# Optimization experiments

Hardware: AMD Instinct MI355X
Metric: run time of the kernel (lower is better)

Reference implementation:

```python
import jax, jax.numpy as jnp
import numpy as np

USER_NUM = 100000
ITEM_NUM = 50000
N_NODES = USER_NUM + ITEM_NUM
HIDE_DIM = 64
N_EDGES = 4000000
LAYER_NUM = 3


def setup_inputs() -> dict:
    key = jax.random.key(0)
    k1, k2, k3, k4 = jax.random.split(key, 4)
    # Xavier uniform for embeddings: bound = sqrt(6/(fan_in+fan_out))
    bound_u = float(np.sqrt(6.0 / (USER_NUM + HIDE_DIM)))
    bound_i = float(np.sqrt(6.0 / (ITEM_NUM + HIDE_DIM)))
    user_emb = jax.random.uniform(k1, (USER_NUM, HIDE_DIM), jnp.float32, -bound_u, bound_u)
    item_emb = jax.random.uniform(k2, (ITEM_NUM, HIDE_DIM), jnp.float32, -bound_i, bound_i)
    src = jax.random.randint(k3, (N_EDGES,), 0, N_NODES, dtype=jnp.int32)
    dst = jax.random.randint(k4, (N_EDGES,), 0, N_NODES, dtype=jnp.int32)
    return {"user_emb": user_emb, "item_emb": item_emb, "src": src, "dst": dst}


def _gcn_layer(node_f, src, dst, out_norm, in_norm):
    # node_f: [N, D]; symmetric degree-normalized SpMM (copy_u + sum)
    h = node_f * out_norm  # pre-scale by out_degree^-0.5
    agg = jax.ops.segment_sum(h[src], dst, num_segments=N_NODES)
    return agg * in_norm  # post-scale by in_degree^-0.5


def reference(user_emb, item_emb, src, dst):
    ones = jnp.ones((N_EDGES,), jnp.float32)
    out_deg = jnp.clip(jax.ops.segment_sum(ones, src, num_segments=N_NODES), 1.0)
    in_deg = jnp.clip(jax.ops.segment_sum(ones, dst, num_segments=N_NODES), 1.0)
    out_norm = (out_deg ** -0.5)[:, None]
    in_norm = (in_deg ** -0.5)[:, None]

    res_user = user_emb
    res_item = item_emb
    for i in range(LAYER_NUM):
        if i == 0:
            node_f = jnp.concatenate([res_user, res_item], axis=0)
        else:
            node_f = embeddings
        embeddings = _gcn_layer(node_f, src, dst, out_norm, in_norm)
        scale = 1.0 / (i + 2)
        res_user = res_user + embeddings[:USER_NUM] * scale
        res_item = res_item + embeddings[USER_NUM:] * scale
    return (res_user, res_item)
```

## Files before the change

kernel.cpp:

```cpp
#include <hip/hip_runtime.h>
#include <stdint.h>

#define USER_NUM 100000
#define ITEM_NUM 50000
#define N_NODES  150000
#define HIDE_DIM 64
#define N_EDGES  4000000

#define HRANGES 3
#define RNODES  50000
#define RWORDS  (RNODES / 4)
#define SLICES  128
#define EPS     (N_EDGES / SLICES)
#define NRB     ((HRANGES * RWORDS + 511) / 512)

#define BSH     9
#define BNODES  512
#define NBUCK   293
#define SSLICES 640
#define EPSB    (N_EDGES / SSLICES)

#define STAGE_CAP 15000
#define INIT_BLOCKS ((N_NODES * 32) / 512)

__device__ __forceinline__ unsigned short f2bf(float f) {
    union { float f; unsigned int i; } c; c.f = f;
    unsigned int b = c.i;
    return (unsigned short)((b + 0x7FFFu + ((b >> 16) & 1u)) >> 16);
}
__device__ __forceinline__ float lo_bf(uint32_t u) {
    union { uint32_t u; float f; } c; c.u = u << 16; return c.f;
}
__device__ __forceinline__ float hi_bf(uint32_t u) {
    union { uint32_t u; float f; } c; c.u = u & 0xffff0000u; return c.f;
}

__global__ void histfused_kernel(const int* __restrict__ src, const int* __restrict__ dst,
                                 uint32_t* __restrict__ partial, uint32_t* __restrict__ btot) {
    __shared__ uint32_t bins[RWORDS];
    int r  = blockIdx.x / SLICES;
    int sl = blockIdx.x - r * SLICES;
    int e0 = sl * EPS, e1 = e0 + EPS;
    if (r < HRANGES) {
        for (int i = threadIdx.x; i < RWORDS; i += 512) bins[i] = 0;
        __syncthreads();
        int lo = r * RNODES, hi = lo + RNODES;
        for (int e = e0 + threadIdx.x; e < e1; e += 512) {
            int s = src[e];
            if (s >= lo && s < hi) {
                int x = s - lo;
                atomicAdd(&bins[x >> 2], 1u << (8 * (x & 3)));
            }
        }
        __syncthreads();
        uint32_t* out = partial + (size_t)(r * SLICES + sl) * RWORDS;
        for (int i = threadIdx.x; i < RWORDS; i += 512) out[i] = bins[i];
    } else {
        for (int i = threadIdx.x; i < NBUCK; i += 512) bins[i] = 0;
        __syncthreads();
        for (int e = e0 + threadIdx.x; e < e1; e += 512)
            atomicAdd(&bins[((unsigned)dst[e]) >> BSH], 1u);
        __syncthreads();
        for (int i = threadIdx.x; i < NBUCK; i += 512)
            if (bins[i]) atomicAdd(&btot[i], bins[i]);
    }
}

__global__ void rednorm_kernel(const uint32_t* __restrict__ partial, float* __restrict__ out_norm,
                               const uint32_t* __restrict__ btot, uint32_t* __restrict__ bbase) {
    if (blockIdx.x == NRB) {
        __shared__ uint32_t tot[512];
        int t = threadIdx.x;
        uint32_t v = (t < NBUCK) ? btot[t] : 0;
        tot[t] = v;
        __syncthreads();
        for (int off = 1; off < 512; off <<= 1) {
            uint32_t x = (t >= off) ? tot[t - off] : 0;
            __syncthreads();
            tot[t] += x;
            __syncthreads();
        }
        if (t < NBUCK) bbase[t] = tot[t] - v;
        if (t == NBUCK - 1) bbase[NBUCK] = tot[t];
        return;
    }
    int g = blockIdx.x * 512 + threadIdx.x;
    if (g >= HRANGES * RWORDS) return;
    int r = g / RWORDS, w = g - r * RWORDS;
    const uint32_t* p = partial + (size_t)r * SLICES * RWORDS + w;
    uint32_t acc = 0;
#pragma unroll 16
    for (int sl = 0; sl < SLICES; ++sl) acc += p[(size_t)sl * RWORDS];
    int oc0 = acc & 255, oc1 = (acc >> 8) & 255, oc2 = (acc >> 16) & 255, oc3 = (acc >> 24);
    float4 o;
    o.x = 1.0f / sqrtf((float)(oc0 < 1 ? 1 : oc0));
    o.y = 1.0f / sqrtf((float)(oc1 < 1 ? 1 : oc1));
    o.z = 1.0f / sqrtf((float)(oc2 < 1 ? 1 : oc2));
    o.w = 1.0f / sqrtf((float)(oc3 < 1 ? 1 : oc3));
    ((float4*)out_norm)[(size_t)r * (RNODES / 4) + w] = o;
}

__global__ void scatter_kernel(const int* __restrict__ src, const int* __restrict__ dst,
                               const uint32_t* __restrict__ bbase, uint32_t* __restrict__ gcur,
                               uint32_t* __restrict__ sorted) {
    __shared__ uint32_t cnt[NBUCK];
    __shared__ uint32_t excl[NBUCK];
    __shared__ uint32_t gpos0[NBUCK];
    __shared__ uint32_t sarr[512];
    __shared__ uint32_t sval[EPSB];
    __shared__ uint16_t sbkt[EPSB];

    int s = blockIdx.x;
    int t = threadIdx.x;
    for (int i = t; i < NBUCK; i += 512) cnt[i] = 0;
    __syncthreads();

    int e0 = s * EPSB;
    for (int e = e0 + t; e < e0 + EPSB; e += 512)
        atomicAdd(&cnt[((unsigned)dst[e]) >> BSH], 1u);
    __syncthreads();

    uint32_t myc = (t < NBUCK) ? cnt[t] : 0;
    sarr[t] = myc;
    __syncthreads();
    for (int off = 1; off < 512; off <<= 1) {
        uint32_t x = (t >= off) ? sarr[t - off] : 0;
        __syncthreads();
        sarr[t] += x;
        __syncthreads();
    }
    if (t < NBUCK) {
        uint32_t ex = sarr[t] - myc;
        excl[t] = ex;
        cnt[t] = ex;
        if (myc) gpos0[t] = bbase[t] + atomicAdd(&gcur[t], myc);
    }
    __syncthreads();

    for (int e = e0 + t; e < e0 + EPSB; e += 512) {
        unsigned d = (unsigned)dst[e];
        int sv = src[e];
        unsigned b = d >> BSH;
        unsigned nib = d & (BNODES - 1);
        uint32_t r = atomicAdd(&cnt[b], 1u);
        sval[r] = (uint32_t)sv | (nib << 18);
        sbkt[r] = (uint16_t)b;
    }
    __syncthreads();

    for (int i = t; i < EPSB; i += 512) {
        unsigned b = sbkt[i];
        sorted[gpos0[b] + ((uint32_t)i - excl[b])] = sval[i];
    }
}

__global__ __launch_bounds__(512) void slabinit_kernel(
        const uint32_t* __restrict__ sorted, const uint32_t* __restrict__ btot,
        const uint32_t* __restrict__ bbase,
        int* __restrict__ esrc, int* __restrict__ in_cnt, float* __restrict__ in_norm,
        uint32_t* __restrict__ rowptr,
        const float2* __restrict__ user2, const float2* __restrict__ item2,
        const float* __restrict__ out_norm, uint32_t* __restrict__ h0) {
    int t = threadIdx.x;
    if (blockIdx.x >= NBUCK) {
        int gid = (blockIdx.x - NBUCK) * 512 + t;
        if (gid < N_NODES * 32) {
            int node = gid >> 5;
            float2 v = (node < USER_NUM) ? user2[gid] : item2[gid - USER_NUM * 32];
            float on = out_norm[node];
            h0[gid] = (uint32_t)f2bf(v.x * on) | ((uint32_t)f2bf(v.y * on) << 16);
        }
        return;
    }
    __shared__ uint32_t cnt[BNODES];
    __shared__ uint32_t sarr[BNODES];
    __shared__ int stage[STAGE_CAP];
    int b = blockIdx.x;
    uint32_t start = bbase[b];
    uint32_t n = btot[b];
    cnt[t] = 0;
    __syncthreads();

    for (uint32_t i = t; i < n; i += 512)
        atomicAdd(&cnt[sorted[start + i] >> 18], 1u);
    __syncthreads();

    uint32_t v = cnt[t];
    sarr[t] = v;
    __syncthreads();
    for (int off = 1; off < 512; off <<= 1) {
        uint32_t x = (t >= off) ? sarr[t - off] : 0;
        __syncthreads();
        sarr[t] += x;
        __syncthreads();
    }
    uint32_t excl = sarr[t] - v;
    int node = (b << BSH) + t;
    if (node < N_NODES) {
        rowptr[node] = start + excl;
        in_cnt[node] = (int)v;
        in_norm[node] = 1.0f / sqrtf((float)(v < 1 ? 1 : v));
    }
    cnt[t] = excl;
    __syncthreads();

    if (n <= STAGE_CAP) {
        for (uint32_t i = t; i < n; i += 512) {
            uint32_t w = sorted[start + i];
            uint32_t r = atomicAdd(&cnt[w >> 18], 1u);
            stage[r] = (int)(w & 0x3FFFFu);
        }
        __syncthreads();
        for (uint32_t i = t; i < n; i += 512) esrc[start + i] = stage[i];
    } else {
        for (uint32_t i = t; i < n; i += 512) {
            uint32_t w = sorted[start + i];
            uint32_t r = atomicAdd(&cnt[w >> 18], 1u);
            esrc[start + r] = (int)(w & 0x3FFFFu);
        }
    }
}

__global__ void agg_kernel(const uint32_t* __restrict__ h32, const int* __restrict__ esrc,
                           const uint32_t* __restrict__ rowptr, const int* __restrict__ in_cnt,
                           const float* __restrict__ in_norm, const float* __restrict__ out_norm,
                           const float4* __restrict__ user4, const float4* __restrict__ item4,
                           float4* __restrict__ res4, uint4* __restrict__ hn128,
                           const uint2* __restrict__ h1own,
                           float s1, float s2, float s3, int mode) {
    int wid  = (blockIdx.x * blockDim.x + threadIdx.x) >> 6;
    int lane = threadIdx.x & 63;
    int half = lane >> 5;
    int p    = (lane >> 3) & 3;
    int q    = lane & 7;
    int node = wid * 2 + half;
    if (node >= N_NODES) return;

    int deg = in_cnt[node];
    int beg = (int)rowptr[node];
    int hb  = half << 5;

    int sl0 = lane & 31;
    int idx0 = (sl0      < deg) ? esrc[beg + sl0]      : 0;
    int idx1 = (sl0 + 32 < deg) ? esrc[beg + sl0 + 32] : 0;

    const uint4* h128 = (const uint4*)h32;

    float a0 = 0.f, a1 = 0.f, a2 = 0.f, a3 = 0.f;
    float a4 = 0.f, a5 = 0.f, a6 = 0.f, a7 = 0.f;

#define ACC8(U) do { \
        a0 += lo_bf((U).x); a1 += hi_bf((U).x); \
        a2 += lo_bf((U).y); a3 += hi_bf((U).y); \
        a4 += lo_bf((U).z); a5 += hi_bf((U).z); \
        a6 += lo_bf((U).w); a7 += hi_bf((U).w); } while (0)

    int d0 = (deg < 32) ? deg : 32;
    {
        int sA0 = __shfl(idx0, hb + p,      64);
        int sA1 = __shfl(idx0, hb + 4 + p,  64);
        int sA2 = __shfl(idx0, hb + 8 + p,  64);
        int sA3 = __shfl(idx0, hb + 12 + p, 64);
        uint4 uA0 = h128[sA0 * 8 + q];
        uint4 uA1 = h128[sA1 * 8 + q];
        uint4 uA2 = h128[sA2 * 8 + q];
        uint4 uA3 = h128[sA3 * 8 + q];
        int sB0 = __shfl(idx0, hb + 16 + p, 64);
        int sB1 = __shfl(idx0, hb + 20 + p, 64);
        int sB2 = __shfl(idx0, hb + 24 + p, 64);
        int sB3 = __shfl(idx0, hb + 28 + p, 64);
        uint4 uB0 = h128[sB0 * 8 + q];
        uint4 uB1 = h128[sB1 * 8 + q];
        uint4 uB2 = h128[sB2 * 8 + q];
        uint4 uB3 = h128[sB3 * 8 + q];
        if (p      < d0) ACC8(uA0);
        if (4 + p  < d0) ACC8(uA1);
        if (8 + p  < d0) ACC8(uA2);
        if (12 + p < d0) ACC8(uA3);
        if (16 + p < d0) ACC8(uB0);
        if (20 + p < d0) ACC8(uB1);
        if (24 + p < d0) ACC8(uB2);
        if (28 + p < d0) ACC8(uB3);
    }

    int m1 = ((deg < 64) ? deg : 64) - 32;
    if (m1 > 0) {
        int nj1 = (m1 + 3) >> 2;
        int j = 0;
        for (; 4 * j + 8 <= m1; j += 2) {
            int e0 = 4 * j + p;
            int s0 = __shfl(idx1, hb + e0,     64);
            int s1g = __shfl(idx1, hb + e0 + 4, 64);
            uint4 u0 = h128[s0 * 8 + q];
            uint4 u1 = h128[s1g * 8 + q];
            ACC8(u0);
            ACC8(u1);
        }
        for (; j < nj1; ++j) {
            int e = 4 * j + p;
            int s = __shfl(idx1, hb + e, 64);
            uint4 u = h128[s * 8 + q];
            if (e < m1) ACC8(u);
        }
    }

    for (int e = 64 + p; e < deg; e += 4) {
        int s = esrc[beg + e];
        uint4 u = h128[s * 8 + q];
        ACC8(u);
    }
#undef ACC8

    a0 += __shfl_xor(a0, 8, 64);  a1 += __shfl_xor(a1, 8, 64);
    a2 += __shfl_xor(a2, 8, 64);  a3 += __shfl_xor(a3, 8, 64);
    a4 += __shfl_xor(a4, 8, 64);  a5 += __shfl_xor(a5, 8, 64);
    a6 += __shfl_xor(a6, 8, 64);  a7 += __shfl_xor(a7, 8, 64);
    a0 += __shfl_xor(a0, 16, 64); a1 += __shfl_xor(a1, 16, 64);
    a2 += __shfl_xor(a2, 16, 64); a3 += __shfl_xor(a3, 16, 64);
    a4 += __shfl_xor(a4, 16, 64); a5 += __shfl_xor(a5, 16, 64);
    a6 += __shfl_xor(a6, 16, 64); a7 += __shfl_xor(a7, 16, 64);

    float innorm = in_norm[node];
    float v0 = a0 * innorm, v1 = a1 * innorm, v2 = a2 * innorm, v3 = a3 * innorm;
    float v4 = a4 * innorm, v5 = a5 * innorm, v6 = a6 * innorm, v7 = a7 * innorm;

    if (mode == 0) {
        if (p == 0) {
            float on = out_norm[node];
            uint4 w;
            w.x = (uint32_t)f2bf(v0 * on) | ((uint32_t)f2bf(v1 * on) << 16);
            w.y = (uint32_t)f2bf(v2 * on) | ((uint32_t)f2bf(v3 * on) << 16);
            w.z = (uint32_t)f2bf(v4 * on) | ((uint32_t)f2bf(v5 * on) << 16);
            w.w = (uint32_t)f2bf(v6 * on) | ((uint32_t)f2bf(v7 * on) << 16);
            hn128[node * 8 + q] = w;
        }
    } else {
        if (p == 1 || p == 2) {
            int of = node * 16 + 2 * q + (p - 1);
            float4 x = (node < USER_NUM) ? user4[of] : item4[of - USER_NUM * 16];
            uint2 h1 = h1own[of];
            uint2 h2 = ((const uint2*)h32)[of];
            float rinv = 1.0f / out_norm[node];
            float b0 = (p == 1) ? v0 : v4;
            float b1 = (p == 1) ? v1 : v5;
            float b2 = (p == 1) ? v2 : v6;
            float b3 = (p == 1) ? v3 : v7;
            float4 rv;
            rv.x = x.x + (lo_bf(h1.x) * s1 + lo_bf(h2.x) * s2) * rinv + b0 * s3;
            rv.y = x.y + (hi_bf(h1.x) * s1 + hi_bf(h2.x) * s2) * rinv + b1 * s3;
            rv.z = x.z + (lo_bf(h1.y) * s1 + lo_bf(h2.y) * s2) * rinv + b2 * s3;
            rv.w = x.w + (hi_bf(h1.y) * s1 + hi_bf(h2.y) * s2) * rinv + b3 * s3;
            res4[of] = rv;
        }
    }
}

static inline uintptr_t align_up(uintptr_t p, uintptr_t a) { return (p + a - 1) & ~(a - 1); }

extern "C" void kernel_launch(void* const* d_in, const int* in_sizes, int n_in,
                              void* d_out, int out_size, void* d_ws, size_t ws_size,
                              hipStream_t stream) {
    const float* user_emb = (const float*)d_in[0];
    const float* item_emb = (const float*)d_in[1];
    const int*   src      = (const int*)d_in[2];
    const int*   dst      = (const int*)d_in[3];
    float*       res      = (float*)d_out;

    uintptr_t p = (uintptr_t)d_ws;
    int* in_cnt = (int*)p;                     p = align_up(p + (size_t)N_NODES * 4, 128);
    float* out_norm = (float*)p;               p = align_up(p + (size_t)N_NODES * 4, 128);
    float* in_norm = (float*)p;                p = align_up(p + (size_t)N_NODES * 4, 128);
    uint32_t* rowptr = (uint32_t*)p;           p = align_up(p + (size_t)N_NODES * 4, 128);
    uint32_t* btot = (uint32_t*)p;             p = align_up(p + (size_t)(2 * NBUCK) * 4, 128);
    uint32_t* bbase = (uint32_t*)p;            p = align_up(p + (size_t)(NBUCK + 1) * 4, 128);
    int* esrc = (int*)p;                       p = align_up(p + (size_t)N_EDGES * 4, 128);
    uint32_t* hA = (uint32_t*)p;               p = align_up(p + (size_t)N_NODES * 32 * 4, 128);
    uint32_t* hB = (uint32_t*)p;
    uint32_t* gcur = btot + NBUCK;
    uint32_t* sorted  = hA;
    uint32_t* partial = hB;

    const int BT = 256;
    int ab = (N_NODES / 2 * 64 + BT - 1) / BT;

    const float2* user2 = (const float2*)user_emb;
    const float2* item2 = (const float2*)item_emb;
    const float4* user4 = (const float4*)user_emb;
    const float4* item4 = (const float4*)item_emb;

    hipMemsetAsync(btot, 0, (size_t)(2 * NBUCK) * 4, stream);
    histfused_kernel<<<(HRANGES + 1) * SLICES, 512, 0, stream>>>(src, dst, partial, btot);
    rednorm_kernel<<<NRB + 1, 512, 0, stream>>>(partial, out_norm, btot, bbase);
    scatter_kernel<<<SSLICES, 512, 0, stream>>>(src, dst, bbase, gcur, sorted);
    slabinit_kernel<<<NBUCK + INIT_BLOCKS, 512, 0, stream>>>(
        sorted, btot, bbase, esrc, in_cnt, in_norm, rowptr, user2, item2, out_norm, hB);

    agg_kernel<<<ab, BT, 0, stream>>>(hB, esrc, rowptr, in_cnt, in_norm, out_norm, user4, item4,
                                      (float4*)res, (uint4*)hA, (const uint2*)hA,
                                      0.0f, 0.0f, 0.0f, 0);
    agg_kernel<<<ab, BT, 0, stream>>>(hA, esrc, rowptr, in_cnt, in_norm, out_norm, user4, item4,
                                      (float4*)res, (uint4*)hB, (const uint2*)hA,
                                      0.0f, 0.0f, 0.0f, 0);
    agg_kernel<<<ab, BT, 0, stream>>>(hB, esrc, rowptr, in_cnt, in_norm, out_norm, user4, item4,
                                      (float4*)res, (uint4*)hA, (const uint2*)hA,
                                      0.5f, 1.0f / 3.0f, 0.25f, 1);
}
```

Measured before the change: 412.9 us.

## Reuse per-slice dst bucket counts from histogram pass in scatter kernel

The dst-bucket histogram blocks now record per-sub-slice bucket counts into a workspace buffer, so the scatter kernel no longer rereads dst and counts buckets itself before its prefix scan. Separately, the src degree histogram uses two node ranges of 75000 instead of three of 50000, which cuts the number of passes over src and the block count. The trade-off is a larger shared histogram per block, which may lower occupancy, and partial-sum buffers that are larger per range. The count buffer borrows the esrc workspace before esrc is written.

```diff
diff --git a/kernel.cpp b/kernel.cpp
--- a/kernel.cpp
+++ b/kernel.cpp
@@ -7,8 +7,8 @@
 #define HIDE_DIM 64
 #define N_EDGES  4000000
 
-#define HRANGES 3
-#define RNODES  50000
+#define HRANGES 2
+#define RNODES  75000
 #define RWORDS  (RNODES / 4)
 #define SLICES  128
 #define EPS     (N_EDGES / SLICES)
@@ -19,6 +19,7 @@
 #define NBUCK   293
 #define SSLICES 640
 #define EPSB    (N_EDGES / SSLICES)
+#define NSUB    (EPS / EPSB)
 
 #define STAGE_CAP 15000
 #define INIT_BLOCKS ((N_NODES * 32) / 512)
@@ -35,8 +36,10 @@
     union { uint32_t u; float f; } c; c.u = u & 0xffff0000u; return c.f;
 }
 
-__global__ void histfused_kernel(const int* __restrict__ src, const int* __restrict__ dst,
-                                 uint32_t* __restrict__ partial, uint32_t* __restrict__ btot) {
+__global__ __launch_bounds__(512) void histfused_kernel(
+        const int* __restrict__ src, const int* __restrict__ dst,
+        uint32_t* __restrict__ partial, uint32_t* __restrict__ btot,
+        uint32_t* __restrict__ cntA) {
     __shared__ uint32_t bins[RWORDS];
     int r  = blockIdx.x / SLICES;
     int sl = blockIdx.x - r * SLICES;
@@ -56,13 +59,23 @@
         uint32_t* out = partial + (size_t)(r * SLICES + sl) * RWORDS;
         for (int i = threadIdx.x; i < RWORDS; i += 512) out[i] = bins[i];
     } else {
-        for (int i = threadIdx.x; i < NBUCK; i += 512) bins[i] = 0;
-        __syncthreads();
-        for (int e = e0 + threadIdx.x; e < e1; e += 512)
-            atomicAdd(&bins[((unsigned)dst[e]) >> BSH], 1u);
-        __syncthreads();
-        for (int i = threadIdx.x; i < NBUCK; i += 512)
-            if (bins[i]) atomicAdd(&btot[i], bins[i]);
+        for (int i = threadIdx.x; i < NSUB * NBUCK; i += 512) bins[i] = 0;
+        __syncthreads();
+        for (int e = e0 + threadIdx.x; e < e1; e += 512) {
+            int sub = (e - e0) / EPSB;
+            atomicAdd(&bins[sub * NBUCK + (((unsigned)dst[e]) >> BSH)], 1u);
+        }
+        __syncthreads();
+        for (int i = threadIdx.x; i < NBUCK; i += 512) {
+            uint32_t tot = 0;
+#pragma unroll
+            for (int sub = 0; sub < NSUB; ++sub) {
+                uint32_t c = bins[sub * NBUCK + i];
+                cntA[(size_t)(sl * NSUB + sub) * NBUCK + i] = c;
+                tot += c;
+            }
+            if (tot) atomicAdd(&btot[i], tot);
+        }
     }
 }
 
@@ -97,12 +110,13 @@
     o.y = 1.0f / sqrtf((float)(oc1 < 1 ? 1 : oc1));
     o.z = 1.0f / sqrtf((float)(oc2 < 1 ? 1 : oc2));
     o.w = 1.0f / sqrtf((float)(oc3 < 1 ? 1 : oc3));
-    ((float4*)out_norm)[(size_t)r * (RNODES / 4) + w] = o;
-}
-
-__global__ void scatter_kernel(const int* __restrict__ src, const int* __restrict__ dst,
-                               const uint32_t* __restrict__ bbase, uint32_t* __restrict__ gcur,
-                               uint32_t* __restrict__ sorted) {
+    ((float4*)out_norm)[(size_t)r * RWORDS + w] = o;
+}
+
+__global__ __launch_bounds__(512) void scatter_kernel(
+        const int* __restrict__ src, const int* __restrict__ dst,
+        const uint32_t* __restrict__ cntA, const uint32_t* __restrict__ bbase,
+        uint32_t* __restrict__ gcur, uint32_t* __restrict__ sorted) {
     __shared__ uint32_t cnt[NBUCK];
     __shared__ uint32_t excl[NBUCK];
     __shared__ uint32_t gpos0[NBUCK];
@@ -112,15 +126,8 @@
 
     int s = blockIdx.x;
     int t = threadIdx.x;
-    for (int i = t; i < NBUCK; i += 512) cnt[i] = 0;
-    __syncthreads();
-
-    int e0 = s * EPSB;
-    for (int e = e0 + t; e < e0 + EPSB; e += 512)
-        atomicAdd(&cnt[((unsigned)dst[e]) >> BSH], 1u);
-    __syncthreads();
-
-    uint32_t myc = (t < NBUCK) ? cnt[t] : 0;
+
+    uint32_t myc = (t < NBUCK) ? cntA[(size_t)s * NBUCK + t] : 0;
     sarr[t] = myc;
     __syncthreads();
     for (int off = 1; off < 512; off <<= 1) {
@@ -137,6 +144,7 @@
     }
     __syncthreads();
 
+    int e0 = s * EPSB;
     for (int e = e0 + t; e < e0 + EPSB; e += 512) {
         unsigned d = (unsigned)dst[e];
         int sv = src[e];
@@ -379,6 +387,7 @@
     uint32_t* gcur = btot + NBUCK;
     uint32_t* sorted  = hA;
     uint32_t* partial = hB;
+    uint32_t* cntA    = (uint32_t*)esrc;
 
     const int BT = 256;
     int ab = (N_NODES / 2 * 64 + BT - 1) / BT;
@@ -389,9 +398,9 @@
     const float4* item4 = (const float4*)item_emb;
 
     hipMemsetAsync(btot, 0, (size_t)(2 * NBUCK) * 4, stream);
-    histfused_kernel<<<(HRANGES + 1) * SLICES, 512, 0, stream>>>(src, dst, partial, btot);
+    histfused_kernel<<<(HRANGES + 1) * SLICES, 512, 0, stream>>>(src, dst, partial, btot, cntA);
     rednorm_kernel<<<NRB + 1, 512, 0, stream>>>(partial, out_norm, btot, bbase);
-    scatter_kernel<<<SSLICES, 512, 0, stream>>>(src, dst, bbase, gcur, sorted);
+    scatter_kernel<<<SSLICES, 512, 0, stream>>>(src, dst, cntA, bbase, gcur, sorted);
     slabinit_kernel<<<NBUCK + INIT_BLOCKS, 512, 0, stream>>>(
         sorted, btot, bbase, esrc, in_cnt, in_norm, rowptr, user2, item2, out_norm, hB);
 
```

After: 412.7 us. No clear change (-0.0%).
